# Kernel tuning notes

Hardware: AMD Instinct MI355X
Metric: run time of the kernel (lower is better)

The kernel has to match this reference:

```python
import jax, jax.numpy as jnp
import numpy as np

N = 100000      # nodes
E = 1600000     # edges (avg degree 16)
DIN = 32        # input feature dim
H = 16          # nhidden
DEPTH = 4       # number of SAGEConv layers


def setup_inputs() -> dict:
    key = jax.random.key(0)
    ks = jax.random.split(key, 16)
    s = 0.1
    inp = {
        "x": jax.random.normal(ks[0], (N, DIN), jnp.float32),
        "edge_index": jax.random.randint(ks[1], (2, E), 0, N, dtype=jnp.int64),
        # SAGEConv layer 0: in=DIN -> out=H. lin_l has bias, lin_r has no bias (PyG default).
        "Wl0": jax.random.normal(ks[2], (H, DIN), jnp.float32) * s,
        "bl0": jnp.zeros((H,), jnp.float32),
        "Wr0": jax.random.normal(ks[3], (H, DIN), jnp.float32) * s,
        # SAGEConv layers 1..3: in=H -> out=H, stacked.
        "Wls": jax.random.normal(ks[4], (DEPTH - 1, H, H), jnp.float32) * s,
        "bls": jnp.zeros((DEPTH - 1, H), jnp.float32),
        "Wrs": jax.random.normal(ks[5], (DEPTH - 1, H, H), jnp.float32) * s,
        # lin_out MLP: [H, 2H, 2H, 1] with acts [silu, silu, None], no batch norm.
        "W1": jax.random.normal(ks[6], (2 * H, H), jnp.float32) * s,
        "b1": jnp.zeros((2 * H,), jnp.float32),
        "W2": jax.random.normal(ks[7], (2 * H, 2 * H), jnp.float32) * s,
        "b2": jnp.zeros((2 * H,), jnp.float32),
        "W3": jax.random.normal(ks[8], (1, 2 * H), jnp.float32) * s,
        "b3": jnp.zeros((1,), jnp.float32),
    }
    return inp


def reference(x, edge_index, Wl0, bl0, Wr0, Wls, bls, Wrs, W1, b1, W2, b2, W3, b3):
    src = edge_index[0]  # message source (x_j)
    dst = edge_index[1]  # aggregation target (x_i)

    def sage(h, Wl, bl, Wr):
        # sum-aggregate neighbor features, then lin_l(agg) + lin_r(h)
        agg = jax.ops.segment_sum(h[src], dst, num_segments=N)  # [N, d]
        return agg @ Wl.T + bl + h @ Wr.T

    x = jax.nn.silu(sage(x, Wl0, bl0, Wr0))
    for i in range(DEPTH - 1):
        x = jax.nn.silu(sage(x, Wls[i], bls[i], Wrs[i]))

    out = jax.nn.silu(x @ W1.T + b1)
    out = jax.nn.silu(out @ W2.T + b2)
    out = out @ W3.T + b3  # [N, 1]
    return out
```

## Files before the change

kernel.cpp:

```cpp
#include <hip/hip_runtime.h>


#define SH      8
#define BWID    256
#define NBK     512
#define CHUNK   2048
#define EPT     (CHUNK / 256)
#define BCAP    5120

__device__ __forceinline__ float silu_f(float v) {
    return v * __builtin_amdgcn_rcpf(1.0f + __expf(-v));
}

__device__ __forceinline__ float bf_lo(unsigned u) { return __uint_as_float(u << 16); }
__device__ __forceinline__ float bf_hi(unsigned u) { return __uint_as_float(u & 0xFFFF0000u); }
__device__ __forceinline__ unsigned short f2bf(float f) {
    unsigned x = __float_as_uint(f);
    unsigned r = x + 0x7FFFu + ((x >> 16) & 1u);
    return (unsigned short)(r >> 16);
}
__device__ __forceinline__ unsigned pack_bf2(float a, float b) {
    return (unsigned)f2bf(a) | ((unsigned)f2bf(b) << 16);
}


__global__ __launch_bounds__(256) void bin_dense0(
    const int* __restrict__ src, const int* __restrict__ dst,
    unsigned short* __restrict__ cnt16,
    unsigned short* __restrict__ scan16,
    unsigned* __restrict__ binned0,
    const float* __restrict__ x,
    const float* __restrict__ Wl0, const float* __restrict__ bl0,
    const float* __restrict__ Wr0,
    unsigned* __restrict__ hlb, float* __restrict__ acc,
    int n, int ne, int nblocks)
{
    __shared__ int      s_hist[NBK];
    __shared__ int      s_off[NBK];
    __shared__ int      s_p[256];
    __shared__ unsigned s_items[CHUNK];
    __shared__ float    sWl[512], sWr[512], sbl[16];

    const int t = threadIdx.x;
    const int blk = blockIdx.x;
    for (int i = t; i < 512; i += 256) { sWl[i] = Wl0[i]; sWr[i] = Wr0[i]; }
    if (t < 16) sbl[t] = bl0[t];

    const int base = blk * CHUNK;
    const int cnt = min(CHUNK, ne - base);

    int es[EPT], ed[EPT];
#pragma unroll
    for (int j = 0; j < EPT; ++j) {
        const int i = t + j * 256;
        if (i < cnt) { es[j] = src[base + i]; ed[j] = dst[base + i]; }
        else         { es[j] = -1; ed[j] = -1; }
    }

    s_hist[t] = 0; s_hist[t + 256] = 0;
    __syncthreads();
#pragma unroll
    for (int j = 0; j < EPT; ++j)
        if (es[j] >= 0) atomicAdd(&s_hist[ed[j] >> SH], 1);
    __syncthreads();

    const int c0 = s_hist[2 * t], c1 = s_hist[2 * t + 1];
    const int ps = c0 + c1;
    s_p[t] = ps;
    __syncthreads();
    int v = ps;
    for (int o = 1; o < 256; o <<= 1) {
        const int add = (t >= o) ? s_p[t - o] : 0;
        __syncthreads();
        v += add;
        s_p[t] = v;
        __syncthreads();
    }
    const int ex = v - ps;
    s_off[2 * t] = ex;
    s_off[2 * t + 1] = ex + c0;

    cnt16[blk * NBK + t]        = (unsigned short)s_hist[t];
    cnt16[blk * NBK + t + 256]  = (unsigned short)s_hist[t + 256];
    s_hist[t] = 0; s_hist[t + 256] = 0;
    __syncthreads();
    scan16[blk * NBK + t]       = (unsigned short)s_off[t];
    scan16[blk * NBK + t + 256] = (unsigned short)s_off[t + 256];

#pragma unroll
    for (int j = 0; j < EPT; ++j) {
        if (es[j] >= 0) {
            const int b  = ed[j] >> SH;
            const int ld = ed[j] & (BWID - 1);
            const int r  = atomicAdd(&s_hist[b], 1);
            s_items[s_off[b] + r] = ((unsigned)ld << 17) | (unsigned)es[j];
        }
    }
    __syncthreads();

    for (int i = t; i < cnt; i += 256)
        binned0[base + i] = s_items[i];

    if (t >= 128) return;
    const int node = blk * 128 + t;
    if (node >= n) return;

    float h[32];
    const float4* __restrict__ xp = (const float4*)(x + (size_t)node * 32);
#pragma unroll
    for (int r = 0; r < 8; ++r) {
        const float4 vv = xp[r];
        h[4*r+0] = vv.x; h[4*r+1] = vv.y; h[4*r+2] = vv.z; h[4*r+3] = vv.w;
    }

    const float4* __restrict__ sWl4 = (const float4*)sWl;
    const float4* __restrict__ sWr4 = (const float4*)sWr;
    float ol[16], oa[16];
#pragma unroll
    for (int j = 0; j < 16; ++j) {
        float al = 0.f, ar = 0.f;
#pragma unroll
        for (int d4 = 0; d4 < 8; ++d4) {
            const float4 wl = sWl4[j * 8 + d4];
            const float4 wr = sWr4[j * 8 + d4];
            al = fmaf(wl.x, h[4*d4+0], al); al = fmaf(wl.y, h[4*d4+1], al);
            al = fmaf(wl.z, h[4*d4+2], al); al = fmaf(wl.w, h[4*d4+3], al);
            ar = fmaf(wr.x, h[4*d4+0], ar); ar = fmaf(wr.y, h[4*d4+1], ar);
            ar = fmaf(wr.z, h[4*d4+2], ar); ar = fmaf(wr.w, h[4*d4+3], ar);
        }
        ol[j] = al;
        oa[j] = sbl[j] + ar;
    }

    unsigned u[8];
#pragma unroll
    for (int r = 0; r < 8; ++r) u[r] = pack_bf2(ol[2*r], ol[2*r+1]);
    uint4* __restrict__ hp = (uint4*)(hlb + (size_t)node * 8);
    hp[0] = make_uint4(u[0], u[1], u[2], u[3]);
    hp[1] = make_uint4(u[4], u[5], u[6], u[7]);
    float4* __restrict__ ap = (float4*)(acc + (size_t)node * 16);
#pragma unroll
    for (int r = 0; r < 4; ++r)
        ap[r] = make_float4(oa[4*r], oa[4*r+1], oa[4*r+2], oa[4*r+3]);
}

__global__ __launch_bounds__(512) void node_sort(
    const unsigned* __restrict__ binned0,
    const unsigned short* __restrict__ cnt16,
    const unsigned short* __restrict__ scan16,
    int* __restrict__ binned1,
    int2* __restrict__ noff2,
    int n, int nblocks)
{
    __shared__ int cnt[BWID];
    __shared__ int off_[BWID];
    const int b = blockIdx.x, t = threadIdx.x;
    const int dbase = b * BCAP;

    if (t < BWID) cnt[t] = 0;
    __syncthreads();

    for (int i = t; i < nblocks; i += 512) {
        const int c = cnt16[i * NBK + b];
        const int s = scan16[i * NBK + b];
        const unsigned* __restrict__ run = binned0 + (size_t)i * CHUNK + s;
        for (int r = 0; r < c; ++r)
            atomicAdd(&cnt[run[r] >> 17], 1);
    }
    __syncthreads();

    if (t < BWID) off_[t] = cnt[t];
    __syncthreads();
    for (int o = 1; o < BWID; o <<= 1) {
        const int add = (t < BWID && t >= o) ? off_[t - o] : 0;
        __syncthreads();
        if (t < BWID) off_[t] += add;
        __syncthreads();
    }
    if (t < BWID) off_[t] -= cnt[t];
    __syncthreads();

    if (t < BWID) {
        const int node = (b << SH) + t;
        if (node < n)
            noff2[node] = make_int2(dbase + off_[t], dbase + off_[t] + cnt[t]);
        cnt[t] = 0;
    }
    __syncthreads();

    for (int i = t; i < nblocks; i += 512) {
        const int c = cnt16[i * NBK + b];
        const int s = scan16[i * NBK + b];
        const unsigned* __restrict__ run = binned0 + (size_t)i * CHUNK + s;
        for (int r = 0; r < c; ++r) {
            const unsigned u = run[r];
            const int ld = (int)(u >> 17);
            const int r2 = atomicAdd(&cnt[ld], 1);
            binned1[dbase + off_[ld] + r2] = (int)(u & 0x1FFFFu);
        }
    }
}


__device__ __forceinline__ void gather16_4(
    const int* __restrict__ binned1, const uint4* __restrict__ h4,
    int beg, int end, int q, float* p)
{
#pragma unroll
    for (int i = 0; i < 16; ++i) p[i] = 0.f;
    int k = beg + q;
    for (; k + 4 < end; k += 8) {
        const int s0 = binned1[k];
        const int s1 = binned1[k + 4];
        const uint4 a0 = h4[(size_t)s0 * 2];
        const uint4 a1 = h4[(size_t)s0 * 2 + 1];
        const uint4 b0 = h4[(size_t)s1 * 2];
        const uint4 b1 = h4[(size_t)s1 * 2 + 1];
        p[0] += bf_lo(a0.x); p[1] += bf_hi(a0.x); p[2] += bf_lo(a0.y); p[3] += bf_hi(a0.y);
        p[4] += bf_lo(a0.z); p[5] += bf_hi(a0.z); p[6] += bf_lo(a0.w); p[7] += bf_hi(a0.w);
        p[8] += bf_lo(a1.x); p[9] += bf_hi(a1.x); p[10]+= bf_lo(a1.y); p[11]+= bf_hi(a1.y);
        p[12]+= bf_lo(a1.z); p[13]+= bf_hi(a1.z); p[14]+= bf_lo(a1.w); p[15]+= bf_hi(a1.w);
        p[0] += bf_lo(b0.x); p[1] += bf_hi(b0.x); p[2] += bf_lo(b0.y); p[3] += bf_hi(b0.y);
        p[4] += bf_lo(b0.z); p[5] += bf_hi(b0.z); p[6] += bf_lo(b0.w); p[7] += bf_hi(b0.w);
        p[8] += bf_lo(b1.x); p[9] += bf_hi(b1.x); p[10]+= bf_lo(b1.y); p[11]+= bf_hi(b1.y);
        p[12]+= bf_lo(b1.z); p[13]+= bf_hi(b1.z); p[14]+= bf_lo(b1.w); p[15]+= bf_hi(b1.w);
    }
    if (k < end) {
        const int s0 = binned1[k];
        const uint4 a0 = h4[(size_t)s0 * 2];
        const uint4 a1 = h4[(size_t)s0 * 2 + 1];
        p[0] += bf_lo(a0.x); p[1] += bf_hi(a0.x); p[2] += bf_lo(a0.y); p[3] += bf_hi(a0.y);
        p[4] += bf_lo(a0.z); p[5] += bf_hi(a0.z); p[6] += bf_lo(a0.w); p[7] += bf_hi(a0.w);
        p[8] += bf_lo(a1.x); p[9] += bf_hi(a1.x); p[10]+= bf_lo(a1.y); p[11]+= bf_hi(a1.y);
        p[12]+= bf_lo(a1.z); p[13]+= bf_hi(a1.z); p[14]+= bf_lo(a1.w); p[15]+= bf_hi(a1.w);
    }
#pragma unroll
    for (int i = 0; i < 16; ++i) p[i] += __shfl_xor(p[i], 1);
#pragma unroll
    for (int i = 0; i < 16; ++i) p[i] += __shfl_xor(p[i], 2);
}

__global__ __launch_bounds__(256, 4) void fused_agg_dense(
    const int2* __restrict__ noff2, const int* __restrict__ binned1,
    const unsigned* __restrict__ hl_in, const float* __restrict__ acc_in,
    const float* __restrict__ Wl, const float* __restrict__ bl,
    const float* __restrict__ Wr,
    unsigned* __restrict__ hl_out, float* __restrict__ acc_out, int n)
{
    __shared__ float sWl[256], sWr[256], sbl[16];
    const int t = threadIdx.x;
    sWl[t] = Wl[t]; sWr[t] = Wr[t];
    if (t < 16) sbl[t] = bl[t];
    __syncthreads();

    const int gid = blockIdx.x * 256 + t;
    const int node = gid >> 2;
    if (node >= n) return;
    const int q = t & 3;
    const int2 be = noff2[node];

    float p[16];
    gather16_4(binned1, (const uint4*)hl_in, be.x, be.y, q, p);

    const float4* __restrict__ ai = (const float4*)(acc_in + (size_t)node * 16);
    float h[16];
#pragma unroll
    for (int r = 0; r < 4; ++r) {
        const float4 a = ai[r];
        h[4*r+0] = silu_f(a.x + p[4*r+0]);
        h[4*r+1] = silu_f(a.y + p[4*r+1]);
        h[4*r+2] = silu_f(a.z + p[4*r+2]);
        h[4*r+3] = silu_f(a.w + p[4*r+3]);
    }

    const float4* __restrict__ sWl4 = (const float4*)sWl;
    const float4* __restrict__ sWr4 = (const float4*)sWr;
    float ol[4], oa[4];
#pragma unroll
    for (int jj = 0; jj < 4; ++jj) {
        const int j = 4 * q + jj;
        float al = 0.f, ar = 0.f;
#pragma unroll
        for (int d4 = 0; d4 < 4; ++d4) {
            const float4 wl = sWl4[j * 4 + d4];
            const float4 wr = sWr4[j * 4 + d4];
            al = fmaf(wl.x, h[4*d4+0], al); al = fmaf(wl.y, h[4*d4+1], al);
            al = fmaf(wl.z, h[4*d4+2], al); al = fmaf(wl.w, h[4*d4+3], al);
            ar = fmaf(wr.x, h[4*d4+0], ar); ar = fmaf(wr.y, h[4*d4+1], ar);
            ar = fmaf(wr.z, h[4*d4+2], ar); ar = fmaf(wr.w, h[4*d4+3], ar);
        }
        ol[jj] = al;
        oa[jj] = sbl[j] + ar;
    }

    ((uint2*)hl_out)[(size_t)node * 4 + q] =
        make_uint2(pack_bf2(ol[0], ol[1]), pack_bf2(ol[2], ol[3]));
    ((float4*)acc_out)[(size_t)node * 4 + q] =
        make_float4(oa[0], oa[1], oa[2], oa[3]);
}

__global__ __launch_bounds__(256, 3) void fused_agg_mlp(
    const int2* __restrict__ noff2, const int* __restrict__ binned1,
    const unsigned* __restrict__ hl_in, const float* __restrict__ acc_in,
    const float* __restrict__ W1, const float* __restrict__ b1,
    const float* __restrict__ W2, const float* __restrict__ b2,
    const float* __restrict__ W3, const float* __restrict__ b3,
    float* __restrict__ out, int n)
{
    __shared__ float sW1[512], sW2[1024], sb1[32], sb2[32], sW3[32];
    __shared__ float sb3;
    const int t = threadIdx.x;
    for (int i = t; i < 512; i += 256) sW1[i] = W1[i];
    for (int i = t; i < 1024; i += 256) sW2[i] = W2[i];
    if (t < 32) { sb1[t] = b1[t]; sb2[t] = b2[t]; sW3[t] = W3[t]; }
    if (t == 0) sb3 = b3[0];
    __syncthreads();

    const int gid = blockIdx.x * 256 + t;
    const int node = gid >> 2;
    if (node >= n) return;
    const int q = t & 3;
    const int2 be = noff2[node];

    float p[16];
    gather16_4(binned1, (const uint4*)hl_in, be.x, be.y, q, p);

    const float4* __restrict__ ai = (const float4*)(acc_in + (size_t)node * 16);
    float h[16];
#pragma unroll
    for (int r = 0; r < 4; ++r) {
        const float4 a = ai[r];
        h[4*r+0] = silu_f(a.x + p[4*r+0]);
        h[4*r+1] = silu_f(a.y + p[4*r+1]);
        h[4*r+2] = silu_f(a.z + p[4*r+2]);
        h[4*r+3] = silu_f(a.w + p[4*r+3]);
    }

    const float4* __restrict__ sW1v = (const float4*)sW1;
    float a1[8];
#pragma unroll
    for (int jj = 0; jj < 8; ++jj) {
        const int j = 8 * q + jj;
        float s = sb1[j];
#pragma unroll
        for (int d4 = 0; d4 < 4; ++d4) {
            const float4 w = sW1v[j * 4 + d4];
            s = fmaf(w.x, h[4*d4+0], s); s = fmaf(w.y, h[4*d4+1], s);
            s = fmaf(w.z, h[4*d4+2], s); s = fmaf(w.w, h[4*d4+3], s);
        }
        a1[jj] = silu_f(s);
    }

    float t0[16];
#pragma unroll
    for (int i = 0; i < 8; ++i) {
        const float mine  = a1[i];
        const float other = __shfl_xor(mine, 1);
        const bool hi = (q & 1);
        t0[i]     = hi ? other : mine;
        t0[8 + i] = hi ? mine  : other;
    }
    float A1[32];
#pragma unroll
    for (int i = 0; i < 16; ++i) {
        const float mine  = t0[i];
        const float other = __shfl_xor(mine, 2);
        const bool hi = (q & 2);
        A1[i]      = hi ? other : mine;
        A1[16 + i] = hi ? mine  : other;
    }

    const float4* __restrict__ sW2v = (const float4*)sW2;
    float part = 0.f;
#pragma unroll
    for (int jj = 0; jj < 8; ++jj) {
        const int j = 8 * q + jj;
        float s = sb2[j];
#pragma unroll
        for (int d4 = 0; d4 < 8; ++d4) {
            const float4 w = sW2v[j * 8 + d4];
            s = fmaf(w.x, A1[4*d4+0], s); s = fmaf(w.y, A1[4*d4+1], s);
            s = fmaf(w.z, A1[4*d4+2], s); s = fmaf(w.w, A1[4*d4+3], s);
        }
        part = fmaf(sW3[j], silu_f(s), part);
    }
    part += __shfl_xor(part, 1);
    part += __shfl_xor(part, 2);
    if (q == 0) out[node] = part + sb3;
}

extern "C" void kernel_launch(void* const* d_in, const int* in_sizes, int n_in,
                              void* d_out, int out_size, void* d_ws, size_t ws_size,
                              hipStream_t stream)
{
    const float* x   = (const float*)d_in[0];
    const int*   ei  = (const int*)d_in[1];
    const float* Wl0 = (const float*)d_in[2];
    const float* bl0 = (const float*)d_in[3];
    const float* Wr0 = (const float*)d_in[4];
    const float* Wls = (const float*)d_in[5];
    const float* bls = (const float*)d_in[6];
    const float* Wrs = (const float*)d_in[7];
    const float* W1  = (const float*)d_in[8];
    const float* b1  = (const float*)d_in[9];
    const float* W2  = (const float*)d_in[10];
    const float* b2  = (const float*)d_in[11];
    const float* W3  = (const float*)d_in[12];
    const float* b3  = (const float*)d_in[13];

    const int n  = in_sizes[0] / 32;
    const int ne = in_sizes[1] / 2;
    const int* src = ei;
    const int* dst = ei + ne;
    const int nbuck   = (n + BWID - 1) >> SH;
    const int nblocks = (ne + CHUNK - 1) / CHUNK;

    float*    acc0    = (float*)d_ws;
    float*    acc1    = acc0 + (size_t)n * 16;
    unsigned* hlbA    = (unsigned*)(acc1 + (size_t)n * 16);
    unsigned* hlbB    = hlbA + (size_t)n * 8;
    int2*     noff2   = (int2*)(hlbB + (size_t)n * 8);
    int*      binned1 = (int*)(noff2 + n);
    unsigned short* cnt16  = (unsigned short*)(binned1 + (size_t)nbuck * BCAP);
    unsigned short* scan16 = cnt16 + (size_t)nblocks * NBK;
    unsigned* binned0 = (unsigned*)(scan16 + (size_t)nblocks * NBK);

    const int lb = (n * 4 + 255) / 256;

    bin_dense0<<<nblocks, 256, 0, stream>>>(src, dst, cnt16, scan16, binned0,
                                            x, Wl0, bl0, Wr0, hlbA, acc0,
                                            n, ne, nblocks);
    node_sort<<<nbuck, 512, 0, stream>>>(binned0, cnt16, scan16, binned1, noff2,
                                         n, nblocks);

    fused_agg_dense<<<lb, 256, 0, stream>>>(noff2, binned1, hlbA, acc0,
        Wls + 0,   bls + 0,  Wrs + 0,   hlbB, acc1, n);
    fused_agg_dense<<<lb, 256, 0, stream>>>(noff2, binned1, hlbB, acc1,
        Wls + 256, bls + 16, Wrs + 256, hlbA, acc0, n);
    fused_agg_dense<<<lb, 256, 0, stream>>>(noff2, binned1, hlbA, acc0,
        Wls + 512, bls + 32, Wrs + 512, hlbB, acc1, n);
    fused_agg_mlp<<<lb, 256, 0, stream>>>(noff2, binned1, hlbB, acc1,
        W1, b1, W2, b2, W3, b3, (float*)d_out, n);
}
```

Measured before the change: 164.0 us.

## Stage bin edges in LDS for node_sort and unroll gather to four edges

node_sort now reads each block's per-chunk counts once, prefix-scans them across threads, and copies all of the bin's edges into shared memory. Both the counting pass and the scatter pass then run over that compact LDS array with all 512 threads instead of serial per-chunk loops. The gather helper now processes four consecutive edges per lane per iteration, giving more independent loads in flight. The cost is a larger LDS footprint, a block-wide scan, and a serial per-thread copy. The new code assumes nblocks <= 2048 and a per-bin total <= BCAP.

New measurement: 155.8 us. 1.05x faster.

```diff
diff --git a/kernel.cpp b/kernel.cpp
--- a/kernel.cpp
+++ b/kernel.cpp
@@ -22,6 +22,12 @@
 __device__ __forceinline__ unsigned pack_bf2(float a, float b) {
     return (unsigned)f2bf(a) | ((unsigned)f2bf(b) << 16);
 }
+
+#define ACC2(u0, u1) \
+    p[0] += bf_lo(u0.x); p[1] += bf_hi(u0.x); p[2] += bf_lo(u0.y); p[3] += bf_hi(u0.y); \
+    p[4] += bf_lo(u0.z); p[5] += bf_hi(u0.z); p[6] += bf_lo(u0.w); p[7] += bf_hi(u0.w); \
+    p[8] += bf_lo(u1.x); p[9] += bf_hi(u1.x); p[10]+= bf_lo(u1.y); p[11]+= bf_hi(u1.y); \
+    p[12]+= bf_lo(u1.z); p[13]+= bf_hi(u1.z); p[14]+= bf_lo(u1.w); p[15]+= bf_hi(u1.w);
 
 
 __global__ __launch_bounds__(256) void bin_dense0(
@@ -152,27 +158,56 @@
     int2* __restrict__ noff2,
     int n, int nblocks)
 {
+    __shared__ unsigned s_edges[BCAP];
     __shared__ int cnt[BWID];
     __shared__ int off_[BWID];
+    __shared__ int s_p[512];
+    __shared__ int s_tot;
     const int b = blockIdx.x, t = threadIdx.x;
     const int dbase = b * BCAP;
 
+    int rc[4], rs[4];
+    int myc = 0;
+#pragma unroll
+    for (int j = 0; j < 4; ++j) {
+        const int i = 4 * t + j;
+        if (i < nblocks) { rc[j] = cnt16[i * NBK + b]; rs[j] = scan16[i * NBK + b]; }
+        else             { rc[j] = 0; rs[j] = 0; }
+        myc += rc[j];
+    }
+    s_p[t] = myc;
+    __syncthreads();
+    int v = myc;
+    for (int o = 1; o < 512; o <<= 1) {
+        const int add = (t >= o) ? s_p[t - o] : 0;
+        __syncthreads();
+        v += add;
+        s_p[t] = v;
+        __syncthreads();
+    }
+    int o = v - myc;
+    if (t == 511) s_tot = v;
     if (t < BWID) cnt[t] = 0;
-    __syncthreads();
-
-    for (int i = t; i < nblocks; i += 512) {
-        const int c = cnt16[i * NBK + b];
-        const int s = scan16[i * NBK + b];
-        const unsigned* __restrict__ run = binned0 + (size_t)i * CHUNK + s;
-        for (int r = 0; r < c; ++r)
-            atomicAdd(&cnt[run[r] >> 17], 1);
-    }
+
+#pragma unroll
+    for (int j = 0; j < 4; ++j) {
+        if (rc[j]) {
+            const unsigned* __restrict__ run =
+                binned0 + (size_t)(4 * t + j) * CHUNK + rs[j];
+            for (int r = 0; r < rc[j]; ++r) s_edges[o++] = run[r];
+        }
+    }
+    __syncthreads();
+    const int tot = s_tot;
+
+    for (int k = t; k < tot; k += 512)
+        atomicAdd(&cnt[s_edges[k] >> 17], 1);
     __syncthreads();
 
     if (t < BWID) off_[t] = cnt[t];
     __syncthreads();
-    for (int o = 1; o < BWID; o <<= 1) {
-        const int add = (t < BWID && t >= o) ? off_[t - o] : 0;
+    for (int o2 = 1; o2 < BWID; o2 <<= 1) {
+        const int add = (t < BWID && t >= o2) ? off_[t - o2] : 0;
         __syncthreads();
         if (t < BWID) off_[t] += add;
         __syncthreads();
@@ -188,16 +223,11 @@
     }
     __syncthreads();
 
-    for (int i = t; i < nblocks; i += 512) {
-        const int c = cnt16[i * NBK + b];
-        const int s = scan16[i * NBK + b];
-        const unsigned* __restrict__ run = binned0 + (size_t)i * CHUNK + s;
-        for (int r = 0; r < c; ++r) {
-            const unsigned u = run[r];
-            const int ld = (int)(u >> 17);
-            const int r2 = atomicAdd(&cnt[ld], 1);
-            binned1[dbase + off_[ld] + r2] = (int)(u & 0x1FFFFu);
-        }
+    for (int k = t; k < tot; k += 512) {
+        const unsigned u = s_edges[k];
+        const int ld = (int)(u >> 17);
+        const int r2 = atomicAdd(&cnt[ld], 1);
+        binned1[dbase + off_[ld] + r2] = (int)(u & 0x1FFFFu);
     }
 }
 
@@ -208,31 +238,24 @@
 {
 #pragma unroll
     for (int i = 0; i < 16; ++i) p[i] = 0.f;
-    int k = beg + q;
-    for (; k + 4 < end; k += 8) {
+    int base = beg;
+    for (; base + 16 <= end; base += 16) {
+        const int k = base + q * 4;
+        const int i0 = binned1[k],     i1 = binned1[k + 1];
+        const int i2 = binned1[k + 2], i3 = binned1[k + 3];
+        const uint4 a0 = h4[(size_t)i0 * 2], a1 = h4[(size_t)i0 * 2 + 1];
+        const uint4 b0 = h4[(size_t)i1 * 2], b1 = h4[(size_t)i1 * 2 + 1];
+        const uint4 c0 = h4[(size_t)i2 * 2], c1 = h4[(size_t)i2 * 2 + 1];
+        const uint4 d0 = h4[(size_t)i3 * 2], d1 = h4[(size_t)i3 * 2 + 1];
+        ACC2(a0, a1)
+        ACC2(b0, b1)
+        ACC2(c0, c1)
+        ACC2(d0, d1)
+    }
+    for (int k = base + q; k < end; k += 4) {
         const int s0 = binned1[k];
-        const int s1 = binned1[k + 4];
-        const uint4 a0 = h4[(size_t)s0 * 2];
-        const uint4 a1 = h4[(size_t)s0 * 2 + 1];
-        const uint4 b0 = h4[(size_t)s1 * 2];
-        const uint4 b1 = h4[(size_t)s1 * 2 + 1];
-        p[0] += bf_lo(a0.x); p[1] += bf_hi(a0.x); p[2] += bf_lo(a0.y); p[3] += bf_hi(a0.y);
-        p[4] += bf_lo(a0.z); p[5] += bf_hi(a0.z); p[6] += bf_lo(a0.w); p[7] += bf_hi(a0.w);
-        p[8] += bf_lo(a1.x); p[9] += bf_hi(a1.x); p[10]+= bf_lo(a1.y); p[11]+= bf_hi(a1.y);
-        p[12]+= bf_lo(a1.z); p[13]+= bf_hi(a1.z); p[14]+= bf_lo(a1.w); p[15]+= bf_hi(a1.w);
-        p[0] += bf_lo(b0.x); p[1] += bf_hi(b0.x); p[2] += bf_lo(b0.y); p[3] += bf_hi(b0.y);
-        p[4] += bf_lo(b0.z); p[5] += bf_hi(b0.z); p[6] += bf_lo(b0.w); p[7] += bf_hi(b0.w);
-        p[8] += bf_lo(b1.x); p[9] += bf_hi(b1.x); p[10]+= bf_lo(b1.y); p[11]+= bf_hi(b1.y);
-        p[12]+= bf_lo(b1.z); p[13]+= bf_hi(b1.z); p[14]+= bf_lo(b1.w); p[15]+= bf_hi(b1.w);
-    }
-    if (k < end) {
-        const int s0 = binned1[k];
-        const uint4 a0 = h4[(size_t)s0 * 2];
-        const uint4 a1 = h4[(size_t)s0 * 2 + 1];
-        p[0] += bf_lo(a0.x); p[1] += bf_hi(a0.x); p[2] += bf_lo(a0.y); p[3] += bf_hi(a0.y);
-        p[4] += bf_lo(a0.z); p[5] += bf_hi(a0.z); p[6] += bf_lo(a0.w); p[7] += bf_hi(a0.w);
-        p[8] += bf_lo(a1.x); p[9] += bf_hi(a1.x); p[10]+= bf_lo(a1.y); p[11]+= bf_hi(a1.y);
-        p[12]+= bf_lo(a1.z); p[13]+= bf_hi(a1.z); p[14]+= bf_lo(a1.w); p[15]+= bf_hi(a1.w);
+        const uint4 a0 = h4[(size_t)s0 * 2], a1 = h4[(size_t)s0 * 2 + 1];
+        ACC2(a0, a1)
     }
 #pragma unroll
     for (int i = 0; i < 16; ++i) p[i] += __shfl_xor(p[i], 1);
```
